# Kernel optimization log

Measured on AMD Instinct MI355X. Metric: run time of the kernel, lower is better.

## Reference

```python
import jax, jax.numpy as jnp
import numpy as np

N_LETTERS = 128
WORD_DIM = 128      # word embed dim; char-LSTM hidden = 64 per direction
SENT_DIM = 256      # sentence embed dim; word-LSTM hidden = 128 per direction
B, S, LW = 128, 64, 16


def _lstm_dir(x, Wih, Whh, b, reverse):
    """One direction of an LSTM. x: [B,T,D], Wih: [4H,D], Whh: [4H,H], b: [4H].
    PyTorch gate order (i, f, g, o). Returns (outputs [B,T,H], final h [B,H])."""
    Bc = x.shape[0]
    H = Whh.shape[-1]
    xw = jnp.einsum('btd,gd->btg', x, Wih) + b  # precompute input projections

    def step(carry, xt):
        h, c = carry
        g = xt + h @ Whh.T
        i, f, gg, o = jnp.split(g, 4, axis=-1)
        c = jax.nn.sigmoid(f) * c + jax.nn.sigmoid(i) * jnp.tanh(gg)
        h = jax.nn.sigmoid(o) * jnp.tanh(c)
        return (h, c), h

    z = jnp.zeros((Bc, H), x.dtype)
    (h, _), hs = jax.lax.scan(step, (z, z), jnp.swapaxes(xw, 0, 1), reverse=reverse)
    return jnp.swapaxes(hs, 0, 1), h


def _bilstm_final(x, Wih_per_layer, Whh, b):
    """2-layer bidirectional LSTM; returns concat of last-layer final hiddens [B,2H].
    Wih_per_layer: list of length 2 of [2,4H,Din_l]; Whh: [2,2,4H,H]; b: [2,2,4H]."""
    hf = hb = None
    for l in range(2):
        of, hf = _lstm_dir(x, Wih_per_layer[l][0], Whh[l, 0], b[l, 0], False)
        ob, hb = _lstm_dir(x, Wih_per_layer[l][1], Whh[l, 1], b[l, 1], True)
        x = jnp.concatenate([of, ob], axis=-1)
    return jnp.concatenate([hf, hb], axis=-1)


def _mlp2(h, W1, b1, W2, b2):
    return jax.nn.relu(h @ W1.T + b1) @ W2.T + b2


def setup_inputs() -> dict:
    rng = np.random.default_rng(0)
    # sentences: non-empty words contiguous at the front of each sentence
    sent_lens = rng.integers(8, S + 1, B)
    word_lens = rng.integers(1, LW + 1, (B, S))
    chars = rng.integers(1, N_LETTERS + 1, (B, S, LW))
    pos = np.arange(LW)
    chars = np.where(pos[None, None, :] < word_lens[:, :, None], chars, 0)
    chars = np.where(np.arange(S)[None, :, None] < sent_lens[:, None, None], chars, 0)
    sentences = jnp.asarray(chars, dtype=jnp.int32)
    # target words: all non-empty (filter in WordEmbedder is then identity)
    wlens = rng.integers(1, LW + 1, B)
    wchars = rng.integers(1, N_LETTERS + 1, (B, LW))
    wchars = np.where(pos[None, :] < wlens[:, None], wchars, 0)
    words = jnp.asarray(wchars, dtype=jnp.int32)

    ks = jax.random.split(jax.random.key(0), 32)
    sc = 0.05
    Hw, Hs = WORD_DIM // 2, SENT_DIM // 2  # 64, 128
    p = {
        'sentences': sentences, 'words': words,
        'emb': jax.random.normal(ks[0], (N_LETTERS + 1, WORD_DIM)) * sc,
        # char-level word LSTM: both layers have input dim WORD_DIM
        'w_Wih': jax.random.normal(ks[1], (2, 2, 4 * Hw, WORD_DIM)) * sc,
        'w_Whh': jax.random.normal(ks[2], (2, 2, 4 * Hw, Hw)) * sc,
        'w_b': jax.random.normal(ks[3], (2, 2, 4 * Hw)) * sc,
        'w_fc_W1': jax.random.normal(ks[4], (WORD_DIM, WORD_DIM)) * sc,
        'w_fc_b1': jax.random.normal(ks[5], (WORD_DIM,)) * sc,
        'w_fc_W2': jax.random.normal(ks[6], (WORD_DIM, WORD_DIM)) * sc,
        'w_fc_b2': jax.random.normal(ks[7], (WORD_DIM,)) * sc,
        # sentence LSTM: layer0 input WORD_DIM, layer1 input SENT_DIM
        's_Wih0': jax.random.normal(ks[8], (2, 4 * Hs, WORD_DIM)) * sc,
        's_Wih1': jax.random.normal(ks[9], (2, 4 * Hs, SENT_DIM)) * sc,
        's_Whh': jax.random.normal(ks[10], (2, 2, 4 * Hs, Hs)) * sc,
        's_b': jax.random.normal(ks[11], (2, 2, 4 * Hs)) * sc,
        's_fc_W1': jax.random.normal(ks[12], (SENT_DIM, SENT_DIM)) * sc,
        's_fc_b1': jax.random.normal(ks[13], (SENT_DIM,)) * sc,
        's_fc_W2': jax.random.normal(ks[14], (SENT_DIM, SENT_DIM)) * sc,
        's_fc_b2': jax.random.normal(ks[15], (SENT_DIM,)) * sc,
        # classifier 384 -> 256 -> 128 -> 2
        'c_W0': jax.random.normal(ks[16], (256, SENT_DIM + WORD_DIM)) * sc,
        'c_b0': jax.random.normal(ks[17], (256,)) * sc,
        'c_W1': jax.random.normal(ks[18], (128, 256)) * sc,
        'c_b1': jax.random.normal(ks[19], (128,)) * sc,
        'c_W2': jax.random.normal(ks[20], (2, 128)) * sc,
        'c_b2': jax.random.normal(ks[21], (2,)) * sc,
    }
    return p


def _word_embed(tokens, emb, w_Wih, w_Whh, w_b, W1, b1, W2, b2):
    x = emb[tokens]  # [N, LW, WORD_DIM]
    h = _bilstm_final(x, [w_Wih[0], w_Wih[1]], w_Whh, w_b)
    return _mlp2(h, W1, b1, W2, b2)


def reference(sentences, words, emb, w_Wih, w_Whh, w_b, w_fc_W1, w_fc_b1,
              w_fc_W2, w_fc_b2, s_Wih0, s_Wih1, s_Whh, s_b, s_fc_W1, s_fc_b1,
              s_fc_W2, s_fc_b2, c_W0, c_b0, c_W1, c_b1, c_W2, c_b2):
    Bc, Sc, Lc = sentences.shape
    flat = sentences.reshape(-1, Lc)
    we = _word_embed(flat, emb, w_Wih, w_Whh, w_b,
                     w_fc_W1, w_fc_b1, w_fc_W2, w_fc_b2)  # [B*S, WORD_DIM]
    # ragged scatter-pad == zero-mask empty word slots (non-empty words are at front)
    nonempty = (flat != 0).any(axis=1)  # [B*S]
    unflat = (we * nonempty[:, None].astype(we.dtype)).reshape(Bc, Sc, WORD_DIM)
    hs = _bilstm_final(unflat, [s_Wih0, s_Wih1], s_Whh, s_b)
    sent_emb = _mlp2(hs, s_fc_W1, s_fc_b1, s_fc_W2, s_fc_b2)  # [B, SENT_DIM]
    word_emb = _word_embed(words, emb, w_Wih, w_Whh, w_b,
                           w_fc_W1, w_fc_b1, w_fc_W2, w_fc_b2)  # [B, WORD_DIM]
    x = jnp.concatenate([sent_emb, word_emb], axis=1)
    x = jax.nn.relu(x @ c_W0.T + c_b0)
    x = jax.nn.relu(x @ c_W1.T + c_b1)
    x = x @ c_W2.T + c_b2
    return jax.nn.log_softmax(x, axis=1)
```

## Files before the change

kernel.cpp:

```cpp
#include <hip/hip_runtime.h>
#include <hip/hip_bf16.h>
#include <math.h>

typedef unsigned int u32;
typedef unsigned short u16;
typedef __hip_bfloat16 bf16_t;
typedef float f32x4 __attribute__((ext_vector_type(4)));
typedef short bf16x8 __attribute__((ext_vector_type(8)));

__device__ __forceinline__ float blo(u32 p){ union{u32 u; float f;} c; c.u = p << 16; return c.f; }
__device__ __forceinline__ float bhi(u32 p){ union{u32 u; float f;} c; c.u = p & 0xFFFF0000u; return c.f; }
#define LOG2E  1.44269504088896340736f
#define LOG2E2 2.88539008177792681472f
__device__ __forceinline__ float fsigm(float x){
  return __builtin_amdgcn_rcpf(1.0f + __builtin_amdgcn_exp2f(-x*LOG2E));
}
__device__ __forceinline__ float ftanh(float x){
  return 1.0f - 2.0f*__builtin_amdgcn_rcpf(1.0f + __builtin_amdgcn_exp2f(x*LOG2E2));
}
__device__ __forceinline__ u16 f2bu(float f){
  union{float f; u32 u;} c; c.f = f;
  u32 u = c.u + 0x7FFFu + ((c.u >> 16) & 1u);
  return (u16)(u >> 16);
}

#define WE_OFF   0u
#define L0O_OFF  2129920u
#define SFIN_OFF 6324224u
#define XW_OFF   6455296u
#define WB_OFF   40009728u
#define SEG_WWIH  0
#define SEG_WWHH  131072
#define SEG_FW1   196608
#define SEG_FW2   212992
#define SEG_SWIH0 229376
#define SEG_SWIH1 360448
#define SEG_SWHH  622592
#define SEG_TOTAL 884736
#define EMB_TOTAL 16512

__global__ __launch_bounds__(256) void prep_weights(
    const float* __restrict__ wWih, const float* __restrict__ wWhh,
    const float* __restrict__ fW1,  const float* __restrict__ fW2,
    const float* __restrict__ sWih0,const float* __restrict__ sWih1,
    const float* __restrict__ sWhh, const float* __restrict__ emb,
    u16* __restrict__ dst, u16* __restrict__ embB)
{
  for (int i = blockIdx.x*256 + threadIdx.x; i < SEG_TOTAL + EMB_TOTAL; i += gridDim.x*256){
    if (i < SEG_TOTAL){
      const float* s; int off;
      if      (i < SEG_WWHH ){ s = wWih;  off = i; }
      else if (i < SEG_FW1  ){ s = wWhh;  off = i - SEG_WWHH; }
      else if (i < SEG_FW2  ){ s = fW1;   off = i - SEG_FW1; }
      else if (i < SEG_SWIH0){ s = fW2;   off = i - SEG_FW2; }
      else if (i < SEG_SWIH1){ s = sWih0; off = i - SEG_SWIH0; }
      else if (i < SEG_SWHH ){ s = sWih1; off = i - SEG_SWIH1; }
      else                   { s = sWhh;  off = i - SEG_SWHH; }
      dst[i] = f2bu(s[off]);
    } else {
      embB[i - SEG_TOTAL] = f2bu(emb[i - SEG_TOTAL]);
    }
  }
}

__global__ __launch_bounds__(512, 2) void word_mfma(
    const int* __restrict__ sentences, const int* __restrict__ words,
    const u16* __restrict__ embB,
    const u16* __restrict__ wWihB, const u16* __restrict__ wWhhB,
    const float* __restrict__ wb,
    const u16* __restrict__ fW1B, const float* __restrict__ fb1,
    const u16* __restrict__ fW2B, const float* __restrict__ fb2,
    bf16_t* __restrict__ we_out )
{
  const int blk  = blockIdx.x;
  const int tid  = threadIdx.x;
  const int lane = tid & 63;
  const int wv   = tid >> 6;
  const int dq   = wv >> 2;
  const int wq   = wv & 3;
  const int lr   = lane & 15;
  const int lg   = lane >> 4;

  __shared__ __align__(16) u16 SQ[16*16*128];
  __shared__ __align__(16) u16 Hb[2][2][16*64];
  __shared__ __align__(16) u16 HF[16*128];
  __shared__ int chs[256];
  __shared__ int emptyf[16];
  u16* A1 = (u16*)Hb;

  const int wbase = blk*16;
  if (tid < 256){
    int w = tid >> 4, t = tid & 15;
    int gw = wbase + w;
    chs[tid] = (gw < 8192) ? sentences[gw*16 + t] : words[(gw - 8192)*16 + t];
  }
  __syncthreads();
  if (tid < 16){
    int acc = 0;
    #pragma unroll
    for (int i = 0; i < 16; ++i) acc |= chs[tid*16 + i];
    emptyf[tid] = (wbase + tid < 8192) && (acc == 0);
  }
  __syncthreads();

  for (int layer = 0; layer < 2; ++layer){
    const int ld = layer*2 + dq;
    bf16x8 bih[4][4], bhh[4][2];
    float bias[4];
    #pragma unroll
    for (int j = 0; j < 4; ++j){
      const int col = (wq + 4*j)*16 + lr;
      bias[j] = wb[ld*256 + col];
      const u16* pih = wWihB + (size_t)(ld*256 + col)*128 + lg*8;
      #pragma unroll
      for (int kk = 0; kk < 4; ++kk) bih[j][kk] = *(const bf16x8*)(pih + kk*32);
      const u16* phh = wWhhB + (size_t)(ld*256 + col)*64 + lg*8;
      #pragma unroll
      for (int kk = 0; kk < 2; ++kk) bhh[j][kk] = *(const bf16x8*)(phh + kk*32);
    }
    float cst[4] = {0.f, 0.f, 0.f, 0.f};
    for (int i = tid; i < 2*2*16*64; i += 512) ((u16*)Hb)[i] = 0;
    __syncthreads();
    int cur = 0;
    bf16x8 xfn[4];
    if (layer == 0){
      const int t0 = dq ? 15 : 0;
      const u16* xp = embB + (size_t)chs[lr*16 + t0]*128 + lg*8;
      #pragma unroll
      for (int kk = 0; kk < 4; ++kk) xfn[kk] = *(const bf16x8*)(xp + kk*32);
    }
    for (int step = 0; step < 16; ++step){
      const int t = dq ? (15 - step) : step;
      f32x4 ac[4];
      #pragma unroll
      for (int j = 0; j < 4; ++j) ac[j] = (f32x4){bias[j], bias[j], bias[j], bias[j]};
      if (layer == 0){
        bf16x8 xf[4];
        #pragma unroll
        for (int kk = 0; kk < 4; ++kk) xf[kk] = xfn[kk];
        if (step < 15){
          const int tn = dq ? (14 - step) : (step + 1);
          const u16* xp = embB + (size_t)chs[lr*16 + tn]*128 + lg*8;
          #pragma unroll
          for (int kk = 0; kk < 4; ++kk) xfn[kk] = *(const bf16x8*)(xp + kk*32);
        }
        #pragma unroll
        for (int kk = 0; kk < 4; ++kk){
          #pragma unroll
          for (int j = 0; j < 4; ++j)
            ac[j] = __builtin_amdgcn_mfma_f32_16x16x32_bf16(xf[kk], bih[j][kk], ac[j], 0, 0, 0);
        }
      } else {
        #pragma unroll
        for (int kk = 0; kk < 4; ++kk){
          const int c = (kk*4 + lg) ^ lr;
          bf16x8 a = *(const bf16x8*)&SQ[((lr*16 + t)*16 + c)*8];
          #pragma unroll
          for (int j = 0; j < 4; ++j)
            ac[j] = __builtin_amdgcn_mfma_f32_16x16x32_bf16(a, bih[j][kk], ac[j], 0, 0, 0);
        }
      }
      #pragma unroll
      for (int kk = 0; kk < 2; ++kk){
        const int c = (kk*4 + lg) ^ (lr & 7);
        bf16x8 a = *(const bf16x8*)&Hb[dq][cur][(lr*8 + c)*8];
        #pragma unroll
        for (int j = 0; j < 4; ++j)
          ac[j] = __builtin_amdgcn_mfma_f32_16x16x32_bf16(a, bhh[j][kk], ac[j], 0, 0, 0);
      }
      const int u = wq*16 + lr;
      #pragma unroll
      for (int r = 0; r < 4; ++r){
        const int w = lg*4 + r;
        float ig = fsigm(ac[0][r]);
        float fg = fsigm(ac[1][r]);
        float gg = ftanh(ac[2][r]);
        float og = fsigm(ac[3][r]);
        cst[r] = fg*cst[r] + ig*gg;
        float hn = og * ftanh(cst[r]);
        u16 hb = f2bu(hn);
        Hb[dq][cur^1][(w*8 + ((u >> 3) ^ (w & 7)))*8 + (u & 7)] = hb;
        const int d = dq*64 + u;
        const int dc = (d >> 3) ^ (w & 15);
        if (layer == 0)       SQ[((w*16 + t)*16 + dc)*8 + (d & 7)] = hb;
        else if (step == 15)  HF[(w*16 + dc)*8 + (d & 7)] = hb;
      }
      __syncthreads();
      cur ^= 1;
    }
  }

  {
    const int col = wv*16 + lr;
    float bs = fb1[col];
    bf16x8 b1[4];
    const u16* src = fW1B + (size_t)col*128 + lg*8;
    #pragma unroll
    for (int kk = 0; kk < 4; ++kk) b1[kk] = *(const bf16x8*)(src + kk*32);
    f32x4 ac = (f32x4){bs, bs, bs, bs};
    #pragma unroll
    for (int kk = 0; kk < 4; ++kk){
      const int c = (kk*4 + lg) ^ lr;
      bf16x8 a = *(const bf16x8*)&HF[(lr*16 + c)*8];
      ac = __builtin_amdgcn_mfma_f32_16x16x32_bf16(a, b1[kk], ac, 0, 0, 0);
    }
    __syncthreads();
    #pragma unroll
    for (int r = 0; r < 4; ++r){
      const int w = lg*4 + r;
      A1[(w*16 + ((col >> 3) ^ (w & 15)))*8 + (col & 7)] = f2bu(fmaxf(ac[r], 0.f));
    }
  }
  __syncthreads();
  {
    const int col = wv*16 + lr;
    float bs = fb2[col];
    bf16x8 b2[4];
    const u16* src = fW2B + (size_t)col*128 + lg*8;
    #pragma unroll
    for (int kk = 0; kk < 4; ++kk) b2[kk] = *(const bf16x8*)(src + kk*32);
    f32x4 ac = (f32x4){bs, bs, bs, bs};
    #pragma unroll
    for (int kk = 0; kk < 4; ++kk){
      const int c = (kk*4 + lg) ^ lr;
      bf16x8 a = *(const bf16x8*)&A1[(lr*16 + c)*8];
      ac = __builtin_amdgcn_mfma_f32_16x16x32_bf16(a, b2[kk], ac, 0, 0, 0);
    }
    u16* wo = (u16*)we_out;
    #pragma unroll
    for (int r = 0; r < 4; ++r){
      const int w = lg*4 + r;
      wo[(size_t)(wbase + w)*128 + col] = emptyf[w] ? (u16)0 : f2bu(ac[r]);
    }
  }
}

template<int KK>
__global__ __launch_bounds__(256, 1) void xw_gemm(
    const u16* __restrict__ X, const u16* __restrict__ W,
    const float* __restrict__ bias, float* __restrict__ out)
{
  const int rowb = blockIdx.x;
  const int colb = blockIdx.y;
  const int tid = threadIdx.x;
  const int lane = tid & 63, wv = tid >> 6;
  const int lr = lane & 15, lg = lane >> 4;
  const int K = KK*32;

  bf16x8 bf[4][KK];
  f32x4 ac[4];
  #pragma unroll
  for (int j = 0; j < 4; ++j){
    const int g = colb*256 + (wv*4 + j)*16 + lr;
    const float bs = bias[g];
    ac[j] = (f32x4){bs, bs, bs, bs};
    const u16* src = W + (size_t)g*K + lg*8;
    #pragma unroll
    for (int kk = 0; kk < KK; ++kk) bf[j][kk] = *(const bf16x8*)(src + kk*32);
  }
  const u16* xr = X + (size_t)(rowb*16 + lr)*K + lg*8;
  #pragma unroll
  for (int kk = 0; kk < KK; ++kk){
    bf16x8 a = *(const bf16x8*)(xr + kk*32);
    #pragma unroll
    for (int j = 0; j < 4; ++j)
      ac[j] = __builtin_amdgcn_mfma_f32_16x16x32_bf16(a, bf[j][kk], ac[j], 0, 0, 0);
  }
  #pragma unroll
  for (int j = 0; j < 4; ++j){
    const int g = colb*256 + (wv*4 + j)*16 + lr;
    #pragma unroll
    for (int r = 0; r < 4; ++r)
      out[(size_t)(rowb*16 + lg*4 + r)*1024 + g] = ac[j][r];
  }
}

__global__ __launch_bounds__(512, 1) void sent_rec(
    const float* __restrict__ xw ,
    const u16* __restrict__ sWhhB ,
    bf16_t* __restrict__ l0out ,
    float* __restrict__ sfin ,
    const int layer)
{
  const int dir = blockIdx.x & 1;
  const int sg0 = (blockIdx.x >> 1) << 4;
  const int tid = threadIdx.x;
  const int lane = tid & 63, wv = tid >> 6;
  const int lr = lane & 15, lg = lane >> 4;

  __shared__ __align__(16) u16 Hs[2][2048];

  bf16x8 bhh[4][4];
  #pragma unroll
  for (int j = 0; j < 4; ++j){
    const int g = (wv + 8*j)*16 + lr;
    const u16* p = sWhhB + (size_t)((layer*2 + dir)*512 + g)*128 + lg*8;
    #pragma unroll
    for (int kk = 0; kk < 4; ++kk) bhh[j][kk] = *(const bf16x8*)(p + kk*32);
  }
  for (int i = tid; i < 4096; i += 512) ((u16*)Hs)[i] = 0;
  float cst[4] = {0.f, 0.f, 0.f, 0.f};

  size_t rowoff[4];
  #pragma unroll
  for (int r = 0; r < 4; ++r)
    rowoff[r] = (size_t)(sg0 + lg*4 + r)*64*1024 + dir*512 + wv*16 + lr;

  float xwv[16], xwn[16];
  {
    const int t0 = dir ? 63 : 0;
    #pragma unroll
    for (int j = 0; j < 4; ++j)
      #pragma unroll
      for (int r = 0; r < 4; ++r)
        xwv[j*4 + r] = xw[rowoff[r] + (size_t)t0*1024 + j*128];
  }
  __syncthreads();

  u16* lob = (u16*)l0out;
  int cur = 0;
  for (int step = 0; step < 64; ++step){
    const int t = dir ? (63 - step) : step;
    f32x4 ac[4];
    #pragma unroll
    for (int j = 0; j < 4; ++j)
      ac[j] = (f32x4){xwv[j*4+0], xwv[j*4+1], xwv[j*4+2], xwv[j*4+3]};
    if (step < 63){
      const int tn = dir ? (62 - step) : (step + 1);
      #pragma unroll
      for (int j = 0; j < 4; ++j)
        #pragma unroll
        for (int r = 0; r < 4; ++r)
          xwn[j*4 + r] = xw[rowoff[r] + (size_t)tn*1024 + j*128];
    }
    #pragma unroll
    for (int kk = 0; kk < 4; ++kk){
      const bf16x8 ha = *(const bf16x8*)&Hs[cur][(lr*16 + ((kk*4 + lg) ^ lr))*8];
      #pragma unroll
      for (int j = 0; j < 4; ++j)
        ac[j] = __builtin_amdgcn_mfma_f32_16x16x32_bf16(ha, bhh[j][kk], ac[j], 0, 0, 0);
    }
    const int u = wv*16 + lr;
    #pragma unroll
    for (int r = 0; r < 4; ++r){
      const int s = lg*4 + r;
      float ig = fsigm(ac[0][r]);
      float fg = fsigm(ac[1][r]);
      float gg = ftanh(ac[2][r]);
      float og = fsigm(ac[3][r]);
      cst[r] = fg*cst[r] + ig*gg;
      float hn = og * ftanh(cst[r]);
      Hs[cur^1][(s*16 + ((u >> 3) ^ s))*8 + (u & 7)] = f2bu(hn);
      if (layer == 0)
        lob[((size_t)(sg0 + s)*64 + t)*256 + dir*128 + u] = f2bu(hn);
      else if (step == 63)
        sfin[(size_t)(sg0 + s)*256 + dir*128 + u] = hn;
    }
    __syncthreads();
    cur ^= 1;
    #pragma unroll
    for (int i = 0; i < 16; ++i) xwv[i] = xwn[i];
  }
}

__global__ __launch_bounds__(256) void head_kernel(
    const float* __restrict__ sfin, const bf16_t* __restrict__ wet,
    const float* __restrict__ sW1, const float* __restrict__ sb1,
    const float* __restrict__ sW2, const float* __restrict__ sb2,
    const float* __restrict__ cW0, const float* __restrict__ cb0,
    const float* __restrict__ cW1, const float* __restrict__ cb1,
    const float* __restrict__ cW2, const float* __restrict__ cb2,
    float* __restrict__ out)
{
  const int bs = blockIdx.x, tid = threadIdx.x;
  __shared__ __align__(16) float hin[256];
  __shared__ __align__(16) float a1[256];
  __shared__ __align__(16) float xcat[384];
  __shared__ __align__(16) float b0o[256];
  __shared__ __align__(16) float h1o[128];
  __shared__ float lg[2];

  hin[tid] = sfin[(size_t)bs*256 + tid];
  if (tid < 64){
    const u32* src = (const u32*)(wet + (size_t)bs*128);
    u32 p = src[tid];
    xcat[256 + tid*2]     = blo(p);
    xcat[256 + tid*2 + 1] = bhi(p);
  }
  __syncthreads();
  {
    const float4* wr = (const float4*)(sW1 + (size_t)tid*256);
    float acc = sb1[tid];
    #pragma unroll
    for (int i = 0; i < 64; ++i){
      float4 v = wr[i]; const float* hp = &hin[i*4];
      acc += hp[0]*v.x + hp[1]*v.y + hp[2]*v.z + hp[3]*v.w;
    }
    a1[tid] = fmaxf(acc, 0.0f);
  }
  __syncthreads();
  {
    const float4* wr = (const float4*)(sW2 + (size_t)tid*256);
    float acc = sb2[tid];
    #pragma unroll
    for (int i = 0; i < 64; ++i){
      float4 v = wr[i]; const float* hp = &a1[i*4];
      acc += hp[0]*v.x + hp[1]*v.y + hp[2]*v.z + hp[3]*v.w;
    }
    xcat[tid] = acc;
  }
  __syncthreads();
  {
    const float4* wr = (const float4*)(cW0 + (size_t)tid*384);
    float acc = cb0[tid];
    #pragma unroll
    for (int i = 0; i < 96; ++i){
      float4 v = wr[i]; const float* hp = &xcat[i*4];
      acc += hp[0]*v.x + hp[1]*v.y + hp[2]*v.z + hp[3]*v.w;
    }
    b0o[tid] = fmaxf(acc, 0.0f);
  }
  __syncthreads();
  if (tid < 128){
    const float4* wr = (const float4*)(cW1 + (size_t)tid*256);
    float acc = cb1[tid];
    #pragma unroll
    for (int i = 0; i < 64; ++i){
      float4 v = wr[i]; const float* hp = &b0o[i*4];
      acc += hp[0]*v.x + hp[1]*v.y + hp[2]*v.z + hp[3]*v.w;
    }
    h1o[tid] = fmaxf(acc, 0.0f);
  }
  __syncthreads();
  if (tid < 2){
    const float4* wr = (const float4*)(cW2 + (size_t)tid*128);
    float acc = cb2[tid];
    #pragma unroll
    for (int i = 0; i < 32; ++i){
      float4 v = wr[i]; const float* hp = &h1o[i*4];
      acc += hp[0]*v.x + hp[1]*v.y + hp[2]*v.z + hp[3]*v.w;
    }
    lg[tid] = acc;
  }
  __syncthreads();
  if (tid == 0){
    float m = fmaxf(lg[0], lg[1]);
    float lse = m + logf(expf(lg[0] - m) + expf(lg[1] - m));
    out[bs*2 + 0] = lg[0] - lse;
    out[bs*2 + 1] = lg[1] - lse;
  }
}

extern "C" void kernel_launch(void* const* d_in, const int* in_sizes, int n_in,
                              void* d_out, int out_size, void* d_ws, size_t ws_size,
                              hipStream_t stream) {
  const int*   sentences = (const int*)d_in[0];
  const int*   words     = (const int*)d_in[1];
  const float* emb    = (const float*)d_in[2];
  const float* wWih   = (const float*)d_in[3];
  const float* wWhh   = (const float*)d_in[4];
  const float* wb     = (const float*)d_in[5];
  const float* fW1    = (const float*)d_in[6];
  const float* fb1    = (const float*)d_in[7];
  const float* fW2    = (const float*)d_in[8];
  const float* fb2    = (const float*)d_in[9];
  const float* sWih0  = (const float*)d_in[10];
  const float* sWih1  = (const float*)d_in[11];
  const float* sWhh   = (const float*)d_in[12];
  const float* sb     = (const float*)d_in[13];
  const float* sW1    = (const float*)d_in[14];
  const float* sb1    = (const float*)d_in[15];
  const float* sW2    = (const float*)d_in[16];
  const float* sb2    = (const float*)d_in[17];
  const float* cW0    = (const float*)d_in[18];
  const float* cb0    = (const float*)d_in[19];
  const float* cW1    = (const float*)d_in[20];
  const float* cb1    = (const float*)d_in[21];
  const float* cW2    = (const float*)d_in[22];
  const float* cb2    = (const float*)d_in[23];

  char* W = (char*)d_ws;
  bf16_t* we   = (bf16_t*)(W + WE_OFF);
  bf16_t* l0o  = (bf16_t*)(W + L0O_OFF);
  float*  sfin = (float*) (W + SFIN_OFF);
  float*  xw   = (float*) (W + XW_OFF);
  u16*    embB = (u16*)   (W + XW_OFF);
  u16*    wB   = (u16*)   (W + WB_OFF);
  bf16_t* wet  = we + (size_t)8192*128;

  prep_weights<<<dim3(440), dim3(256), 0, stream>>>(
      wWih, wWhh, fW1, fW2, sWih0, sWih1, sWhh, emb, wB, embB);
  word_mfma<<<dim3(520), dim3(512), 0, stream>>>(
      sentences, words, embB,
      wB + SEG_WWIH, wB + SEG_WWHH, wb,
      wB + SEG_FW1, fb1, wB + SEG_FW2, fb2, we);
  xw_gemm<4><<<dim3(512, 4), dim3(256), 0, stream>>>(
      (const u16*)we, wB + SEG_SWIH0, sb, xw);
  sent_rec<<<dim3(16), dim3(512), 0, stream>>>(xw, wB + SEG_SWHH, l0o, sfin, 0);
  xw_gemm<8><<<dim3(512, 4), dim3(256), 0, stream>>>(
      (const u16*)l0o, wB + SEG_SWIH1, sb + 1024, xw);
  sent_rec<<<dim3(16), dim3(512), 0, stream>>>(xw, wB + SEG_SWHH, l0o, sfin, 1);
  head_kernel<<<dim3(128), dim3(256), 0, stream>>>(
      sfin, wet, sW1, sb1, sW2, sb2, cW0, cb0, cW1, cb1, cW2, cb2,
      (float*)d_out);
}
```

Before: 382.1 us.

## Skip char-LSTM blocks for all-empty words and deepen xw prefetch in sentence recurrence

The char-LSTM kernel now checks whether all 16 words in a block are empty sentence slots. If so, it writes zeros to the output embedding and returns early, skipping both LSTM layers and the MLP for padding words. The sentence recurrence kernel now prefetches input projections two steps ahead using two alternating register buffers, unrolled by two, which hides global load latency over a longer window. The skip relies on empty slots being masked to zero later, and the deeper prefetch adds register pressure.

```diff
diff --git a/kernel.cpp b/kernel.cpp
--- a/kernel.cpp
+++ b/kernel.cpp
@@ -4,6 +4,7 @@
 
 typedef unsigned int u32;
 typedef unsigned short u16;
+typedef unsigned long long u64;
 typedef __hip_bfloat16 bf16_t;
 typedef float f32x4 __attribute__((ext_vector_type(4)));
 typedef short bf16x8 __attribute__((ext_vector_type(8)));
@@ -102,6 +103,17 @@
     emptyf[tid] = (wbase + tid < 8192) && (acc == 0);
   }
   __syncthreads();
+
+  {
+    int allz = 1;
+    #pragma unroll
+    for (int i = 0; i < 16; ++i) allz &= emptyf[i];
+    if (allz){
+      u64* wo = (u64*)(we_out + (size_t)wbase*128);
+      wo[tid] = 0ull;
+      return;
+    }
+  }
 
   for (int layer = 0; layer < 2; ++layer){
     const int ld = layer*2 + dq;
@@ -275,6 +287,49 @@
   }
 }
 
+#define REC_STEP(S, XV)                                                      \
+  {                                                                          \
+    const int t = dir ? (63 - (S)) : (S);                                    \
+    f32x4 ac[4];                                                             \
+    _Pragma("unroll")                                                        \
+    for (int j = 0; j < 4; ++j)                                              \
+      ac[j] = (f32x4){XV[j*4+0], XV[j*4+1], XV[j*4+2], XV[j*4+3]};           \
+    if ((S) + 2 < 64){                                                       \
+      const int tp = dir ? (63 - ((S)+2)) : ((S)+2);                         \
+      _Pragma("unroll")                                                      \
+      for (int j = 0; j < 4; ++j){                                           \
+        _Pragma("unroll")                                                    \
+        for (int r = 0; r < 4; ++r)                                          \
+          XV[j*4 + r] = xw[rowoff[r] + (size_t)tp*1024 + j*128];             \
+      }                                                                      \
+    }                                                                        \
+    _Pragma("unroll")                                                        \
+    for (int kk = 0; kk < 4; ++kk){                                          \
+      const bf16x8 ha = *(const bf16x8*)&Hs[cur][(lr*16 + ((kk*4 + lg) ^ lr))*8]; \
+      _Pragma("unroll")                                                      \
+      for (int j = 0; j < 4; ++j)                                            \
+        ac[j] = __builtin_amdgcn_mfma_f32_16x16x32_bf16(ha, bhh[j][kk], ac[j], 0, 0, 0); \
+    }                                                                        \
+    const int u = wv*16 + lr;                                                \
+    _Pragma("unroll")                                                        \
+    for (int r = 0; r < 4; ++r){                                             \
+      const int s = lg*4 + r;                                                \
+      float ig = fsigm(ac[0][r]);                                            \
+      float fg = fsigm(ac[1][r]);                                            \
+      float gg = ftanh(ac[2][r]);                                            \
+      float og = fsigm(ac[3][r]);                                            \
+      cst[r] = fg*cst[r] + ig*gg;                                            \
+      float hn = og * ftanh(cst[r]);                                         \
+      Hs[cur^1][(s*16 + ((u >> 3) ^ s))*8 + (u & 7)] = f2bu(hn);             \
+      if (layer == 0)                                                        \
+        lob[((size_t)(sg0 + s)*64 + t)*256 + dir*128 + u] = f2bu(hn);        \
+      else if ((S) == 63)                                                    \
+        sfin[(size_t)(sg0 + s)*256 + dir*128 + u] = hn;                      \
+    }                                                                        \
+    __syncthreads();                                                         \
+    cur ^= 1;                                                                \
+  }
+
 __global__ __launch_bounds__(512, 1) void sent_rec(
     const float* __restrict__ xw ,
     const u16* __restrict__ sWhhB ,
@@ -306,60 +361,25 @@
   for (int r = 0; r < 4; ++r)
     rowoff[r] = (size_t)(sg0 + lg*4 + r)*64*1024 + dir*512 + wv*16 + lr;
 
-  float xwv[16], xwn[16];
-  {
-    const int t0 = dir ? 63 : 0;
+  float xwA[16], xwB[16];
+  {
+    const int tA = dir ? 63 : 0;
+    const int tB = dir ? 62 : 1;
     #pragma unroll
     for (int j = 0; j < 4; ++j)
       #pragma unroll
-      for (int r = 0; r < 4; ++r)
-        xwv[j*4 + r] = xw[rowoff[r] + (size_t)t0*1024 + j*128];
+      for (int r = 0; r < 4; ++r){
+        xwA[j*4 + r] = xw[rowoff[r] + (size_t)tA*1024 + j*128];
+        xwB[j*4 + r] = xw[rowoff[r] + (size_t)tB*1024 + j*128];
+      }
   }
   __syncthreads();
 
   u16* lob = (u16*)l0out;
   int cur = 0;
-  for (int step = 0; step < 64; ++step){
-    const int t = dir ? (63 - step) : step;
-    f32x4 ac[4];
-    #pragma unroll
-    for (int j = 0; j < 4; ++j)
-      ac[j] = (f32x4){xwv[j*4+0], xwv[j*4+1], xwv[j*4+2], xwv[j*4+3]};
-    if (step < 63){
-      const int tn = dir ? (62 - step) : (step + 1);
-      #pragma unroll
-      for (int j = 0; j < 4; ++j)
-        #pragma unroll
-        for (int r = 0; r < 4; ++r)
-          xwn[j*4 + r] = xw[rowoff[r] + (size_t)tn*1024 + j*128];
-    }
-    #pragma unroll
-    for (int kk = 0; kk < 4; ++kk){
-      const bf16x8 ha = *(const bf16x8*)&Hs[cur][(lr*16 + ((kk*4 + lg) ^ lr))*8];
-      #pragma unroll
-      for (int j = 0; j < 4; ++j)
-        ac[j] = __builtin_amdgcn_mfma_f32_16x16x32_bf16(ha, bhh[j][kk], ac[j], 0, 0, 0);
-    }
-    const int u = wv*16 + lr;
-    #pragma unroll
-    for (int r = 0; r < 4; ++r){
-      const int s = lg*4 + r;
-      float ig = fsigm(ac[0][r]);
-      float fg = fsigm(ac[1][r]);
-      float gg = ftanh(ac[2][r]);
-      float og = fsigm(ac[3][r]);
-      cst[r] = fg*cst[r] + ig*gg;
-      float hn = og * ftanh(cst[r]);
-      Hs[cur^1][(s*16 + ((u >> 3) ^ s))*8 + (u & 7)] = f2bu(hn);
-      if (layer == 0)
-        lob[((size_t)(sg0 + s)*64 + t)*256 + dir*128 + u] = f2bu(hn);
-      else if (step == 63)
-        sfin[(size_t)(sg0 + s)*256 + dir*128 + u] = hn;
-    }
-    __syncthreads();
-    cur ^= 1;
-    #pragma unroll
-    for (int i = 0; i < 16; ++i) xwv[i] = xwn[i];
+  for (int s2 = 0; s2 < 64; s2 += 2){
+    REC_STEP(s2,     xwA);
+    REC_STEP(s2 + 1, xwB);
   }
 }
 
```

Measured after the change: 392.7 us. 2.8% more time.

## Batch xw prefetch and layer-0 output stores in 8-step groups; skip all-empty word blocks

Applied to the files above, without the earlier changes.

The sentence LSTM recurrence now loads the input projections for eight timesteps at once and defers the layer-0 hidden-state global stores until the end of each group. This takes global memory traffic out of the per-step critical path between barriers. Separately, the char-LSTM kernel exits early and writes zeros when all 16 words in a block are empty, skipping recurrence work for padding. The grouping costs extra registers (8x16 floats plus buffered outputs), which could lower occupancy or cause spills.

```diff
diff --git a/kernel.cpp b/kernel.cpp
--- a/kernel.cpp
+++ b/kernel.cpp
@@ -4,6 +4,7 @@
 
 typedef unsigned int u32;
 typedef unsigned short u16;
+typedef unsigned long long u64;
 typedef __hip_bfloat16 bf16_t;
 typedef float f32x4 __attribute__((ext_vector_type(4)));
 typedef short bf16x8 __attribute__((ext_vector_type(8)));
@@ -103,6 +104,17 @@
   }
   __syncthreads();
 
+  {
+    int allz = 1;
+    #pragma unroll
+    for (int i = 0; i < 16; ++i) allz &= emptyf[i];
+    if (allz){
+      u64* wo = (u64*)(we_out + (size_t)wbase*128);
+      wo[tid] = 0ull;
+      return;
+    }
+  }
+
   for (int layer = 0; layer < 2; ++layer){
     const int ld = layer*2 + dq;
     bf16x8 bih[4][4], bhh[4][2];
@@ -301,65 +313,70 @@
   for (int i = tid; i < 4096; i += 512) ((u16*)Hs)[i] = 0;
   float cst[4] = {0.f, 0.f, 0.f, 0.f};
 
-  size_t rowoff[4];
+  const float* xb[4];
   #pragma unroll
   for (int r = 0; r < 4; ++r)
-    rowoff[r] = (size_t)(sg0 + lg*4 + r)*64*1024 + dir*512 + wv*16 + lr;
-
-  float xwv[16], xwn[16];
-  {
-    const int t0 = dir ? 63 : 0;
-    #pragma unroll
-    for (int j = 0; j < 4; ++j)
-      #pragma unroll
-      for (int r = 0; r < 4; ++r)
-        xwv[j*4 + r] = xw[rowoff[r] + (size_t)t0*1024 + j*128];
-  }
-  __syncthreads();
-
+    xb[r] = xw + (size_t)(sg0 + lg*4 + r)*64*1024 + dir*512 + wv*16 + lr;
+  const int u = wv*16 + lr;
   u16* lob = (u16*)l0out;
+  __syncthreads();
+
   int cur = 0;
-  for (int step = 0; step < 64; ++step){
-    const int t = dir ? (63 - step) : step;
-    f32x4 ac[4];
-    #pragma unroll
-    for (int j = 0; j < 4; ++j)
-      ac[j] = (f32x4){xwv[j*4+0], xwv[j*4+1], xwv[j*4+2], xwv[j*4+3]};
-    if (step < 63){
-      const int tn = dir ? (62 - step) : (step + 1);
+  for (int g8 = 0; g8 < 8; ++g8){
+    const int s0 = g8*8;
+    float xws[8][16];
+    #pragma unroll
+    for (int s8 = 0; s8 < 8; ++s8){
+      const int t = dir ? (63 - (s0 + s8)) : (s0 + s8);
       #pragma unroll
       for (int j = 0; j < 4; ++j)
         #pragma unroll
         for (int r = 0; r < 4; ++r)
-          xwn[j*4 + r] = xw[rowoff[r] + (size_t)tn*1024 + j*128];
-    }
-    #pragma unroll
-    for (int kk = 0; kk < 4; ++kk){
-      const bf16x8 ha = *(const bf16x8*)&Hs[cur][(lr*16 + ((kk*4 + lg) ^ lr))*8];
+          xws[s8][j*4 + r] = xb[r][(size_t)t*1024 + j*128];
+    }
+    u16 hs8[8][4];
+    #pragma unroll
+    for (int s8 = 0; s8 < 8; ++s8){
+      f32x4 ac[4];
       #pragma unroll
       for (int j = 0; j < 4; ++j)
-        ac[j] = __builtin_amdgcn_mfma_f32_16x16x32_bf16(ha, bhh[j][kk], ac[j], 0, 0, 0);
-    }
-    const int u = wv*16 + lr;
-    #pragma unroll
-    for (int r = 0; r < 4; ++r){
-      const int s = lg*4 + r;
-      float ig = fsigm(ac[0][r]);
-      float fg = fsigm(ac[1][r]);
-      float gg = ftanh(ac[2][r]);
-      float og = fsigm(ac[3][r]);
-      cst[r] = fg*cst[r] + ig*gg;
-      float hn = og * ftanh(cst[r]);
-      Hs[cur^1][(s*16 + ((u >> 3) ^ s))*8 + (u & 7)] = f2bu(hn);
-      if (layer == 0)
-        lob[((size_t)(sg0 + s)*64 + t)*256 + dir*128 + u] = f2bu(hn);
-      else if (step == 63)
-        sfin[(size_t)(sg0 + s)*256 + dir*128 + u] = hn;
-    }
-    __syncthreads();
-    cur ^= 1;
-    #pragma unroll
-    for (int i = 0; i < 16; ++i) xwv[i] = xwn[i];
+        ac[j] = (f32x4){xws[s8][j*4+0], xws[s8][j*4+1], xws[s8][j*4+2], xws[s8][j*4+3]};
+      #pragma unroll
+      for (int kk = 0; kk < 4; ++kk){
+        const bf16x8 ha = *(const bf16x8*)&Hs[cur][(lr*16 + ((kk*4 + lg) ^ lr))*8];
+        #pragma unroll
+        for (int j = 0; j < 4; ++j)
+          ac[j] = __builtin_amdgcn_mfma_f32_16x16x32_bf16(ha, bhh[j][kk], ac[j], 0, 0, 0);
+      }
+      #pragma unroll
+      for (int r = 0; r < 4; ++r){
+        const int s = lg*4 + r;
+        float ig = fsigm(ac[0][r]);
+        float fg = fsigm(ac[1][r]);
+        float gg = ftanh(ac[2][r]);
+        float og = fsigm(ac[3][r]);
+        cst[r] = fg*cst[r] + ig*gg;
+        float hn = og * ftanh(cst[r]);
+        u16 hb = f2bu(hn);
+        hs8[s8][r] = hb;
+        Hs[cur^1][(s*16 + ((u >> 3) ^ s))*8 + (u & 7)] = hb;
+        if (layer == 1 && (s0 + s8) == 63)
+          sfin[(size_t)(sg0 + s)*256 + dir*128 + u] = hn;
+      }
+      __syncthreads();
+      cur ^= 1;
+    }
+    if (layer == 0){
+      #pragma unroll
+      for (int s8 = 0; s8 < 8; ++s8){
+        const int t = dir ? (63 - (s0 + s8)) : (s0 + s8);
+        #pragma unroll
+        for (int r = 0; r < 4; ++r){
+          const int s = lg*4 + r;
+          lob[((size_t)(sg0 + s)*64 + t)*256 + dir*128 + u] = hs8[s8][r];
+        }
+      }
+    }
   }
 }
 
```

After: 405.3 us. +6.1%, slower.

## Reorder xw projections into per-thread contiguous layout and skip all-empty word blocks

Applied to the files above, without the earlier changes.

The xw_gemm output is written in a blocked layout that matches the sent_rec thread mapping, so each thread fetches its 16 gate pre-activations per timestep as four contiguous float4 loads instead of 16 strided scalar loads. This targets the latency-bound serial recurrence, where each step waits on global loads. The word kernel also returns early and writes zeros when all 16 words in a block are empty padding, skipping the char-LSTM for padded sentence slots. The GEMM store becomes more scattered, and the zero write assumes 512 threads times 8 bytes covers exactly 16x128 bf16 outputs.

```diff
diff --git a/kernel.cpp b/kernel.cpp
--- a/kernel.cpp
+++ b/kernel.cpp
@@ -4,6 +4,7 @@
 
 typedef unsigned int u32;
 typedef unsigned short u16;
+typedef unsigned long long u64;
 typedef __hip_bfloat16 bf16_t;
 typedef float f32x4 __attribute__((ext_vector_type(4)));
 typedef short bf16x8 __attribute__((ext_vector_type(8)));
@@ -102,6 +103,17 @@
     emptyf[tid] = (wbase + tid < 8192) && (acc == 0);
   }
   __syncthreads();
+
+  {
+    int allz = 1;
+    #pragma unroll
+    for (int i = 0; i < 16; ++i) allz &= emptyf[i];
+    if (allz){
+      u64* wo = (u64*)(we_out + (size_t)wbase*128);
+      wo[tid] = 0ull;
+      return;
+    }
+  }
 
   for (int layer = 0; layer < 2; ++layer){
     const int ld = layer*2 + dq;
@@ -269,14 +281,22 @@
   #pragma unroll
   for (int j = 0; j < 4; ++j){
     const int g = colb*256 + (wv*4 + j)*16 + lr;
-    #pragma unroll
-    for (int r = 0; r < 4; ++r)
-      out[(size_t)(rowb*16 + lg*4 + r)*1024 + g] = ac[j][r];
+    const int dirq = g >> 9, gd = g & 511;
+    const int cwv = (gd >> 4) & 7, cj = gd >> 7, clr = gd & 15;
+    #pragma unroll
+    for (int r = 0; r < 4; ++r){
+      const int row = rowb*16 + lg*4 + r;
+      const int s = row >> 6, t = row & 63;
+      const int b = ((s >> 4) << 1) | dirq;
+      const int clg = (s >> 2) & 3, cr = s & 3;
+      out[(size_t)b*524288 + (size_t)t*8192
+          + (size_t)((cwv*64 + clg*16 + clr)*16 + cj*4 + cr)] = ac[j][r];
+    }
   }
 }
 
 __global__ __launch_bounds__(512, 1) void sent_rec(
-    const float* __restrict__ xw ,
+    const float* __restrict__ xwc ,
     const u16* __restrict__ sWhhB ,
     bf16_t* __restrict__ l0out ,
     float* __restrict__ sfin ,
@@ -301,38 +321,31 @@
   for (int i = tid; i < 4096; i += 512) ((u16*)Hs)[i] = 0;
   float cst[4] = {0.f, 0.f, 0.f, 0.f};
 
-  size_t rowoff[4];
-  #pragma unroll
-  for (int r = 0; r < 4; ++r)
-    rowoff[r] = (size_t)(sg0 + lg*4 + r)*64*1024 + dir*512 + wv*16 + lr;
-
-  float xwv[16], xwn[16];
+  const float* xb = xwc + (size_t)blockIdx.x*524288 + (size_t)tid*16;
+  const int u = wv*16 + lr;
+  u16* lob = (u16*)l0out;
+
+  float4 xa0, xa1, xa2, xa3, xn0, xn1, xn2, xn3;
   {
     const int t0 = dir ? 63 : 0;
-    #pragma unroll
-    for (int j = 0; j < 4; ++j)
-      #pragma unroll
-      for (int r = 0; r < 4; ++r)
-        xwv[j*4 + r] = xw[rowoff[r] + (size_t)t0*1024 + j*128];
-  }
-  __syncthreads();
-
-  u16* lob = (u16*)l0out;
+    const float4* p = (const float4*)(xb + (size_t)t0*8192);
+    xa0 = p[0]; xa1 = p[1]; xa2 = p[2]; xa3 = p[3];
+  }
+  __syncthreads();
+
   int cur = 0;
   for (int step = 0; step < 64; ++step){
     const int t = dir ? (63 - step) : step;
-    f32x4 ac[4];
-    #pragma unroll
-    for (int j = 0; j < 4; ++j)
-      ac[j] = (f32x4){xwv[j*4+0], xwv[j*4+1], xwv[j*4+2], xwv[j*4+3]};
     if (step < 63){
       const int tn = dir ? (62 - step) : (step + 1);
-      #pragma unroll
-      for (int j = 0; j < 4; ++j)
-        #pragma unroll
-        for (int r = 0; r < 4; ++r)
-          xwn[j*4 + r] = xw[rowoff[r] + (size_t)tn*1024 + j*128];
-    }
+      const float4* p = (const float4*)(xb + (size_t)tn*8192);
+      xn0 = p[0]; xn1 = p[1]; xn2 = p[2]; xn3 = p[3];
+    }
+    f32x4 ac[4];
+    ac[0] = (f32x4){xa0.x, xa0.y, xa0.z, xa0.w};
+    ac[1] = (f32x4){xa1.x, xa1.y, xa1.z, xa1.w};
+    ac[2] = (f32x4){xa2.x, xa2.y, xa2.z, xa2.w};
+    ac[3] = (f32x4){xa3.x, xa3.y, xa3.z, xa3.w};
     #pragma unroll
     for (int kk = 0; kk < 4; ++kk){
       const bf16x8 ha = *(const bf16x8*)&Hs[cur][(lr*16 + ((kk*4 + lg) ^ lr))*8];
@@ -340,7 +353,6 @@
       for (int j = 0; j < 4; ++j)
         ac[j] = __builtin_amdgcn_mfma_f32_16x16x32_bf16(ha, bhh[j][kk], ac[j], 0, 0, 0);
     }
-    const int u = wv*16 + lr;
     #pragma unroll
     for (int r = 0; r < 4; ++r){
       const int s = lg*4 + r;
@@ -350,16 +362,16 @@
       float og = fsigm(ac[3][r]);
       cst[r] = fg*cst[r] + ig*gg;
       float hn = og * ftanh(cst[r]);
-      Hs[cur^1][(s*16 + ((u >> 3) ^ s))*8 + (u & 7)] = f2bu(hn);
+      u16 hb = f2bu(hn);
+      Hs[cur^1][(s*16 + ((u >> 3) ^ s))*8 + (u & 7)] = hb;
       if (layer == 0)
-        lob[((size_t)(sg0 + s)*64 + t)*256 + dir*128 + u] = f2bu(hn);
+        lob[((size_t)(sg0 + s)*64 + t)*256 + dir*128 + u] = hb;
       else if (step == 63)
         sfin[(size_t)(sg0 + s)*256 + dir*128 + u] = hn;
     }
     __syncthreads();
     cur ^= 1;
-    #pragma unroll
-    for (int i = 0; i < 16; ++i) xwv[i] = xwn[i];
+    xa0 = xn0; xa1 = xn1; xa2 = xn2; xa3 = xn3;
   }
 }
 
@@ -483,7 +495,7 @@
   bf16_t* we   = (bf16_t*)(W + WE_OFF);
   bf16_t* l0o  = (bf16_t*)(W + L0O_OFF);
   float*  sfin = (float*) (W + SFIN_OFF);
-  float*  xw   = (float*) (W + XW_OFF);
+  float*  xwc  = (float*) (W + XW_OFF);
   u16*    embB = (u16*)   (W + XW_OFF);
   u16*    wB   = (u16*)   (W + WB_OFF);
   bf16_t* wet  = we + (size_t)8192*128;
@@ -495,11 +507,11 @@
       wB + SEG_WWIH, wB + SEG_WWHH, wb,
       wB + SEG_FW1, fb1, wB + SEG_FW2, fb2, we);
   xw_gemm<4><<<dim3(512, 4), dim3(256), 0, stream>>>(
-      (const u16*)we, wB + SEG_SWIH0, sb, xw);
-  sent_rec<<<dim3(16), dim3(512), 0, stream>>>(xw, wB + SEG_SWHH, l0o, sfin, 0);
+      (const u16*)we, wB + SEG_SWIH0, sb, xwc);
+  sent_rec<<<dim3(16), dim3(512), 0, stream>>>(xwc, wB + SEG_SWHH, l0o, sfin, 0);
   xw_gemm<8><<<dim3(512, 4), dim3(256), 0, stream>>>(
-      (const u16*)l0o, wB + SEG_SWIH1, sb + 1024, xw);
-  sent_rec<<<dim3(16), dim3(512), 0, stream>>>(xw, wB + SEG_SWHH, l0o, sfin, 1);
+      (const u16*)l0o, wB + SEG_SWIH1, sb + 1024, xwc);
+  sent_rec<<<dim3(16), dim3(512), 0, stream>>>(xwc, wB + SEG_SWHH, l0o, sfin, 1);
   head_kernel<<<dim3(128), dim3(256), 0, stream>>>(
       sfin, wet, sW1, sb1, sW2, sb2, cW0, cb0, cW1, cb1, cW2, cb2,
       (float*)d_out);
```

Result: slower. 435.0 us (+13.8%).
